# Kernel optimization log

Hardware: AMD Instinct MI355X
Metric: run time of the kernel (lower is better)

Reference implementation:

```python
import jax, jax.numpy as jnp
import numpy as np

MOMENTUM = 0.9
BN_EPS = 1e-5
NORM_EPS = 1e-12
NUM_CLASSES = 10000
DIM_MLP = 512
NUM_EXPERTS = 3
FEAT_DIM = 256
N = 4096


def _l2norm(x, axis=-1):
    # F.normalize: x / max(||x||, eps)
    n = jnp.sqrt(jnp.sum(x * x, axis=axis, keepdims=True))
    return x / jnp.maximum(n, NORM_EPS)


def setup_inputs() -> dict:
    key = jax.random.key(0)
    ks = jax.random.split(key, 8)
    feat_in = jax.random.normal(ks[0], (N, DIM_MLP * NUM_EXPERTS), dtype=jnp.float32)
    label = jax.random.randint(ks[1], (N,), 0, NUM_CLASSES, dtype=jnp.int32)
    # encoder params
    W1 = jax.random.normal(ks[2], (DIM_MLP * NUM_EXPERTS, DIM_MLP), dtype=jnp.float32) / np.sqrt(DIM_MLP * NUM_EXPERTS)
    b1 = jnp.zeros((DIM_MLP,), dtype=jnp.float32)
    gamma = jnp.ones((DIM_MLP,), dtype=jnp.float32)
    beta = jnp.zeros((DIM_MLP,), dtype=jnp.float32)
    W2 = jax.random.normal(ks[3], (DIM_MLP, FEAT_DIM), dtype=jnp.float32) / np.sqrt(DIM_MLP)
    b2 = jnp.zeros((FEAT_DIM,), dtype=jnp.float32)
    # memory bank buffer: randn then row-normalized (as in __init__)
    memory_pt = _l2norm(jax.random.normal(ks[4], (NUM_CLASSES, FEAT_DIM), dtype=jnp.float32))
    return {"feat_in": feat_in, "label": label, "W1": W1, "b1": b1,
            "gamma": gamma, "beta": beta, "W2": W2, "b2": b2,
            "memory_pt": memory_pt}


def _encoder(feat_in, W1, b1, gamma, beta, W2, b2):
    h = feat_in @ W1 + b1                       # [N, dim_mlp]
    # BatchNorm1d in training mode: batch statistics (biased variance)
    mu = jnp.mean(h, axis=0)
    var = jnp.mean((h - mu) ** 2, axis=0)
    h = (h - mu) * jax.lax.rsqrt(var + BN_EPS) * gamma + beta
    h = jax.nn.relu(h)
    out = h @ W2 + b2                           # [N, 256]
    return _l2norm(out, axis=1)


def _update_memory(memory_pt, feat, label):
    # Strictly sequential per-sample momentum update (order matters for
    # duplicate labels), each touched row renormalized — lax.scan recurrence.
    def step(mem, xy):
        x, y = xy
        pt = MOMENTUM * mem[y] + (1.0 - MOMENTUM) * x
        pt = _l2norm(pt, axis=0)
        return mem.at[y].set(pt), None
    mem, _ = jax.lax.scan(step, memory_pt, (feat, label))
    return mem


def reference(feat_in, label, W1, b1, gamma, beta, W2, b2, memory_pt):
    feat = _encoder(feat_in, W1, b1, gamma, beta, W2, b2)   # [N, 256], unit rows
    # memory_pt.detach(): no grad flows through the memory bank
    mem = _update_memory(jax.lax.stop_gradient(memory_pt),
                         jax.lax.stop_gradient(feat), label)
    mem = jax.lax.stop_gradient(mem)
    sim_logit = jnp.einsum('nc,kc->nk', feat, mem)          # [N, K]
    return sim_logit
```

## Files before the change

kernel.cpp:

```cpp
#include <hip/hip_runtime.h>
#include <stdint.h>

typedef _Float16 f16;
typedef _Float16 f16x2 __attribute__((ext_vector_type(2)));
typedef _Float16 f16x4 __attribute__((ext_vector_type(4)));
typedef _Float16 f16x8 __attribute__((ext_vector_type(8)));
typedef float f32x4 __attribute__((ext_vector_type(4)));

typedef __attribute__((address_space(1))) void gvoid;
typedef __attribute__((address_space(3))) void lvoid;

#define NROWS 4096
#define DIMIN 1536
#define DMLP 512
#define FDIM 256
#define NCLS 10000
#define NPAD 10112
#define NBMW 320

__device__ __forceinline__ void load_lds16(const void* g, void* l) {
    __builtin_amdgcn_global_load_lds((gvoid*)g, (lvoid*)l, 16, 0, 0);
}

template<int TM, int TN, bool STATS, bool NT>
__global__ __launch_bounds__(256) void gemm_t(
    const f16* __restrict__ A, const f16* __restrict__ Bt,
    float* __restrict__ C, const float* __restrict__ bias,
    int K, int ldc, int Nstore,
    float* __restrict__ sums, float* __restrict__ sqs)
{
    constexpr int BK = 64;
    constexpr int AM = TM / 32;
    constexpr int AN = TN / 32;
    constexpr int CA = TM * 8;
    constexpr int CB = TN * 8;
    constexpr int RTOT = (CA + CB) / 256;
    constexpr int SPAN = (TM + TN) * BK;
    static_assert(CA % 256 == 0, "A/B staging split must be round-aligned");

    __shared__ f16 smem[2 * SPAN];

    const int tid  = threadIdx.x;
    const int lane = tid & 63;
    const int w    = tid >> 6;
    const int wm   = (w >> 1) * (TM / 2);
    const int wn   = (w & 1) * (TN / 2);
    const int row0 = blockIdx.x * TM;
    const int col0 = blockIdx.y * TN;
    const int quad = lane >> 4;
    const int r16  = lane & 15;

    f32x4 acc[AM][AN] = {};

    const f16* gsrc[RTOT];
    int ldsoff[RTOT];
#pragma unroll
    for (int r = 0; r < RTOT; ++r) {
        int c = tid + r * 256;
        bool isA = (c < CA);
        int cc = isA ? c : c - CA;
        int row = cc >> 3;
        int gs = (cc & 7) ^ (row & 7);
        gsrc[r] = (isA ? A + (size_t)(row0 + row) * K
                       : Bt + (size_t)(col0 + row) * K) + gs * 8;
        ldsoff[r] = (isA ? 0 : TM * BK) + cc * 8;
    }

    const int nt = K / BK;

#pragma unroll
    for (int r = 0; r < RTOT; ++r)
        load_lds16(gsrc[r], smem + ldsoff[r]);
    __syncthreads();

    int buf = 0;
    for (int t = 0; t < nt; ++t) {
        if (t + 1 < nt) {
            const int k0 = (t + 1) * BK;
            const int o = (buf ^ 1) * SPAN;
#pragma unroll
            for (int r = 0; r < RTOT; ++r)
                load_lds16(gsrc[r] + k0, smem + o + ldsoff[r]);
        }
        const f16* As = smem + buf * SPAN;
        const f16* Bs = As + TM * BK;
#pragma unroll
        for (int ks = 0; ks < 2; ++ks) {
            f16x8 af[AM], bq[AN];
#pragma unroll
            for (int mi = 0; mi < AM; ++mi) {
                int row = wm + mi * 16 + r16;
                int slot = (ks * 4 + quad) ^ (r16 & 7);
                af[mi] = *(const f16x8*)&As[row * BK + slot * 8];
            }
#pragma unroll
            for (int ni = 0; ni < AN; ++ni) {
                int row = wn + ni * 16 + r16;
                int slot = (ks * 4 + quad) ^ (r16 & 7);
                bq[ni] = *(const f16x8*)&Bs[row * BK + slot * 8];
            }
#pragma unroll
            for (int mi = 0; mi < AM; ++mi)
#pragma unroll
                for (int ni = 0; ni < AN; ++ni)
                    acc[mi][ni] = __builtin_amdgcn_mfma_f32_16x16x32_f16(
                        af[mi], bq[ni], acc[mi][ni], 0, 0, 0);
        }
        __syncthreads();
        buf ^= 1;
    }

#pragma unroll
    for (int ni = 0; ni < AN; ++ni) {
        int col = col0 + wn + ni * 16 + r16;
        float bv = bias ? bias[col] : 0.0f;
        float s = 0.0f, q = 0.0f;
        if (col < Nstore) {
#pragma unroll
            for (int mi = 0; mi < AM; ++mi) {
                int rowb = row0 + wm + mi * 16 + quad * 4;
#pragma unroll
                for (int r = 0; r < 4; ++r) {
                    float v = acc[mi][ni][r] + bv;
                    if constexpr (NT)
                        __builtin_nontemporal_store(v, &C[(size_t)(rowb + r) * ldc + col]);
                    else
                        C[(size_t)(rowb + r) * ldc + col] = v;
                    if constexpr (STATS) { s += v; q += v * v; }
                }
            }
        }
        if constexpr (STATS) {
            s += __shfl_xor(s, 16); s += __shfl_xor(s, 32);
            q += __shfl_xor(q, 16); q += __shfl_xor(q, 32);
            if (quad == 0) {
                atomicAdd(&sums[col], s);
                atomicAdd(&sqs[col], q);
            }
        }
    }
}

__global__ void zero_k(float* __restrict__ p, int n) {
    int i = blockIdx.x * 256 + threadIdx.x;
    if (i < n) p[i] = 0.0f;
}

__global__ void f32_to_f16_k(const float* __restrict__ in, f16* __restrict__ out, int n4) {
    int i = blockIdx.x * 256 + threadIdx.x;
    if (i >= n4) return;
    float4 v = *(const float4*)&in[(size_t)i * 4];
    f16x4 o = {(f16)v.x, (f16)v.y, (f16)v.z, (f16)v.w};
    *(f16x4*)&out[(size_t)i * 4] = o;
}

__global__ void transpose_f16_tile_k(const float* __restrict__ in, f16* __restrict__ out,
                                     int R, int C) {
    __shared__ float t[32][33];
    int tx = threadIdx.x & 31, ty = threadIdx.x >> 5;
    int c0 = blockIdx.x * 32, r0 = blockIdx.y * 32;
#pragma unroll
    for (int k = 0; k < 4; ++k)
        t[ty + k * 8][tx] = in[(size_t)(r0 + ty + k * 8) * C + c0 + tx];
    __syncthreads();
#pragma unroll
    for (int k = 0; k < 4; ++k)
        out[(size_t)(c0 + ty + k * 8) * R + r0 + tx] = (f16)t[tx][ty + k * 8];
}

__global__ void touch_k(const int* __restrict__ label, unsigned int* __restrict__ bm) {
    int i = blockIdx.x * 256 + threadIdx.x;
    int y = label[i];
    atomicOr(&bm[y >> 5], 1u << (y & 31));
}

__global__ void bn_finish_k(const float* __restrict__ sums, const float* __restrict__ sqs,
                            const float* __restrict__ gamma, const float* __restrict__ beta,
                            float* __restrict__ scale, float* __restrict__ shift) {
    int c = blockIdx.x * 256 + threadIdx.x;
    if (c >= DMLP) return;
    const float inv_n = 1.0f / 4096.0f;
    float mu = sums[c] * inv_n;
    float var = fmaxf(sqs[c] * inv_n - mu * mu, 0.0f);
    float a = rsqrtf(var + 1e-5f) * gamma[c];
    scale[c] = a;
    shift[c] = beta[c] - mu * a;
}

__global__ void bn_apply_k(const float* __restrict__ h, const float* __restrict__ scale,
                           const float* __restrict__ shift, f16* __restrict__ out) {
    int i = blockIdx.x * 256 + threadIdx.x;
    int c = (i & 127) * 4;
    float4 v = *(const float4*)&h[(size_t)i * 4];
    float4 sc = *(const float4*)&scale[c];
    float4 sh = *(const float4*)&shift[c];
    f16x4 o = {(f16)fmaxf(v.x * sc.x + sh.x, 0.0f),
               (f16)fmaxf(v.y * sc.y + sh.y, 0.0f),
               (f16)fmaxf(v.z * sc.z + sh.z, 0.0f),
               (f16)fmaxf(v.w * sc.w + sh.w, 0.0f)};
    *(f16x4*)&out[(size_t)i * 4] = o;
}

__global__ void l2norm_k(const float* __restrict__ X, float* __restrict__ Y, f16* __restrict__ Yh) {
    int wv = (blockIdx.x * 256 + threadIdx.x) >> 6;
    int lane = threadIdx.x & 63;
    float4 v = *(const float4*)&X[(size_t)wv * FDIM + lane * 4];
    float s = v.x * v.x + v.y * v.y + v.z * v.z + v.w * v.w;
#pragma unroll
    for (int off = 32; off > 0; off >>= 1) s += __shfl_xor(s, off);
    float inv = 1.0f / fmaxf(sqrtf(s), 1e-12f);
    float4 o = {v.x * inv, v.y * inv, v.z * inv, v.w * inv};
    *(float4*)&Y[(size_t)wv * FDIM + lane * 4] = o;
    f16x4 oh = {(f16)o.x, (f16)o.y, (f16)o.z, (f16)o.w};
    *(f16x4*)&Yh[(size_t)wv * FDIM + lane * 4] = oh;
}

__global__ void chain_k(const int* __restrict__ label, const float* __restrict__ feat,
                        const float* __restrict__ mp, const unsigned int* __restrict__ bm,
                        f16* __restrict__ memh) {
    int y = (blockIdx.x * 256 + threadIdx.x) >> 6;
    int lane = threadIdx.x & 63;
    float4 m = {0.f, 0.f, 0.f, 0.f};
    if (y < NCLS) {
        m = *(const float4*)&mp[(size_t)y * FDIM + lane * 4];
        if ((bm[y >> 5] >> (y & 31)) & 1u) {
            for (int g = 0; g < 64; ++g) {
                int lab = label[g * 64 + lane];
                unsigned long long mask = __ballot(lab == y);
                while (mask) {
                    int b = __builtin_ctzll(mask);
                    mask &= mask - 1;
                    int i = g * 64 + b;
                    float4 x = *(const float4*)&feat[(size_t)i * FDIM + lane * 4];
                    m.x = 0.9f * m.x + 0.1f * x.x;
                    m.y = 0.9f * m.y + 0.1f * x.y;
                    m.z = 0.9f * m.z + 0.1f * x.z;
                    m.w = 0.9f * m.w + 0.1f * x.w;
                    float s = m.x * m.x + m.y * m.y + m.z * m.z + m.w * m.w;
#pragma unroll
                    for (int off = 32; off > 0; off >>= 1) s += __shfl_xor(s, off);
                    float inv = 1.0f / fmaxf(sqrtf(s), 1e-12f);
                    m.x *= inv; m.y *= inv; m.z *= inv; m.w *= inv;
                }
            }
        }
    }
    f16x4 o = {(f16)m.x, (f16)m.y, (f16)m.z, (f16)m.w};
    *(f16x4*)&memh[(size_t)y * FDIM + lane * 4] = o;
}

extern "C" void kernel_launch(void* const* d_in, const int* in_sizes, int n_in,
                              void* d_out, int out_size, void* d_ws, size_t ws_size,
                              hipStream_t stream) {
    const float* feat_in = (const float*)d_in[0];
    const int*   label   = (const int*)d_in[1];
    const float* W1      = (const float*)d_in[2];
    const float* b1      = (const float*)d_in[3];
    const float* gamma   = (const float*)d_in[4];
    const float* beta    = (const float*)d_in[5];
    const float* W2      = (const float*)d_in[6];
    const float* b2      = (const float*)d_in[7];
    const float* mp      = (const float*)d_in[8];
    float* out = (float*)d_out;

    char* w = (char*)d_ws;
    f16* A1h   = (f16*)w;   w += (size_t)NROWS * DIMIN * 2;
    f16* W1t   = (f16*)w;   w += (size_t)DMLP * DIMIN * 2;
    f16* W2t   = (f16*)w;   w += (size_t)FDIM * DMLP * 2;
    float* h   = (float*)w; w += (size_t)NROWS * DMLP * 4;
    f16* h2    = (f16*)w;   w += (size_t)NROWS * DMLP * 2;
    float* out2= (float*)w; w += (size_t)NROWS * FDIM * 4;
    float* feat= (float*)w; w += (size_t)NROWS * FDIM * 4;
    f16* feath = (f16*)w;   w += (size_t)NROWS * FDIM * 2;
    f16* memh  = (f16*)w;   w += (size_t)NPAD * FDIM * 2;
    float* sums= (float*)w; w += DMLP * 4;
    float* sqs = (float*)w; w += DMLP * 4;
    unsigned int* bm = (unsigned int*)w; w += NBMW * 4;
    float* bnsc= (float*)w; w += DMLP * 4;
    float* bnsh= (float*)w; w += DMLP * 4;

    zero_k<<<6, 256, 0, stream>>>(sums, 2 * DMLP + NBMW);
    touch_k<<<NROWS / 256, 256, 0, stream>>>(label, bm);
    f32_to_f16_k<<<(NROWS * DIMIN / 4) / 256, 256, 0, stream>>>(feat_in, A1h, NROWS * DIMIN / 4);
    {
        dim3 g1(DMLP / 32, DIMIN / 32);
        transpose_f16_tile_k<<<g1, 256, 0, stream>>>(W1, W1t, DIMIN, DMLP);
        dim3 g2(FDIM / 32, DMLP / 32);
        transpose_f16_tile_k<<<g2, 256, 0, stream>>>(W2, W2t, DMLP, FDIM);
    }

    {
        dim3 g(NROWS / 128, DMLP / 64);
        gemm_t<128, 64, true, false><<<g, 256, 0, stream>>>(
            A1h, W1t, h, b1, DIMIN, DMLP, DMLP, sums, sqs);
    }

    bn_finish_k<<<2, 256, 0, stream>>>(sums, sqs, gamma, beta, bnsc, bnsh);
    bn_apply_k<<<(NROWS * DMLP / 4) / 256, 256, 0, stream>>>(h, bnsc, bnsh, h2);

    {
        dim3 g(NROWS / 64, FDIM / 64);
        gemm_t<64, 64, false, false><<<g, 256, 0, stream>>>(
            h2, W2t, out2, b2, DMLP, FDIM, FDIM, nullptr, nullptr);
    }

    l2norm_k<<<NROWS / 4, 256, 0, stream>>>(out2, feat, feath);

    chain_k<<<NPAD / 4, 256, 0, stream>>>(label, feat, mp, bm, memh);

    {
        dim3 g(NROWS / 128, NPAD / 128);
        gemm_t<128, 128, false, true><<<g, 256, 0, stream>>>(
            feath, memh, out, nullptr, FDIM, NCLS, NCLS, nullptr, nullptr);
    }
}
```

Measured before the change: 295.1 us.

## Fuse setup kernels, fold BN finish into apply, vectorize final GEMM stores

Merges the zeroing, label-bitmap, f32-to-f16 conversion and both weight transposes into one multi-role setup kernel, with the bitmap built in LDS. Folds the BN scale/shift computation into the apply kernel, dropping one launch and a small buffer. Swaps the MFMA operand order in the large similarity GEMM so each lane holds four consecutive columns, allowing 16-byte vector nontemporal stores instead of scalar strided ones. The single-block bitmap role serializes the 4096 label atomics in one workgroup, and the per-thread BN stat recomputation adds some redundant math.

Result: no change. 293.3 us (-0.6%).

```diff
diff --git a/kernel.cpp b/kernel.cpp
--- a/kernel.cpp
+++ b/kernel.cpp
@@ -2,7 +2,6 @@
 #include <stdint.h>
 
 typedef _Float16 f16;
-typedef _Float16 f16x2 __attribute__((ext_vector_type(2)));
 typedef _Float16 f16x4 __attribute__((ext_vector_type(4)));
 typedef _Float16 f16x8 __attribute__((ext_vector_type(8)));
 typedef float f32x4 __attribute__((ext_vector_type(4)));
@@ -22,7 +21,7 @@
     __builtin_amdgcn_global_load_lds((gvoid*)g, (lvoid*)l, 16, 0, 0);
 }
 
-template<int TM, int TN, bool STATS, bool NT>
+template<int TM, int TN, bool STATS, bool NT, bool SWAP>
 __global__ __launch_bounds__(256) void gemm_t(
     const f16* __restrict__ A, const f16* __restrict__ Bt,
     float* __restrict__ C, const float* __restrict__ bias,
@@ -37,6 +36,7 @@
     constexpr int RTOT = (CA + CB) / 256;
     constexpr int SPAN = (TM + TN) * BK;
     static_assert(CA % 256 == 0, "A/B staging split must be round-aligned");
+    static_assert(!(SWAP && STATS), "SWAP epilogue has no STATS path");
 
     __shared__ f16 smem[2 * SPAN];
 
@@ -102,98 +102,145 @@
 #pragma unroll
             for (int mi = 0; mi < AM; ++mi)
 #pragma unroll
-                for (int ni = 0; ni < AN; ++ni)
-                    acc[mi][ni] = __builtin_amdgcn_mfma_f32_16x16x32_f16(
-                        af[mi], bq[ni], acc[mi][ni], 0, 0, 0);
+                for (int ni = 0; ni < AN; ++ni) {
+                    if constexpr (SWAP)
+                        acc[mi][ni] = __builtin_amdgcn_mfma_f32_16x16x32_f16(
+                            bq[ni], af[mi], acc[mi][ni], 0, 0, 0);
+                    else
+                        acc[mi][ni] = __builtin_amdgcn_mfma_f32_16x16x32_f16(
+                            af[mi], bq[ni], acc[mi][ni], 0, 0, 0);
+                }
         }
         __syncthreads();
         buf ^= 1;
     }
 
-#pragma unroll
-    for (int ni = 0; ni < AN; ++ni) {
-        int col = col0 + wn + ni * 16 + r16;
-        float bv = bias ? bias[col] : 0.0f;
-        float s = 0.0f, q = 0.0f;
-        if (col < Nstore) {
-#pragma unroll
-            for (int mi = 0; mi < AM; ++mi) {
-                int rowb = row0 + wm + mi * 16 + quad * 4;
-#pragma unroll
-                for (int r = 0; r < 4; ++r) {
-                    float v = acc[mi][ni][r] + bv;
+    if constexpr (SWAP) {
+#pragma unroll
+        for (int ni = 0; ni < AN; ++ni) {
+            int c0 = col0 + wn + ni * 16 + quad * 4;
+            if (c0 < Nstore) {
+#pragma unroll
+                for (int mi = 0; mi < AM; ++mi) {
+                    int m = row0 + wm + mi * 16 + r16;
                     if constexpr (NT)
-                        __builtin_nontemporal_store(v, &C[(size_t)(rowb + r) * ldc + col]);
+                        __builtin_nontemporal_store(acc[mi][ni],
+                            (f32x4*)&C[(size_t)m * ldc + c0]);
                     else
-                        C[(size_t)(rowb + r) * ldc + col] = v;
-                    if constexpr (STATS) { s += v; q += v * v; }
-                }
-            }
-        }
-        if constexpr (STATS) {
-            s += __shfl_xor(s, 16); s += __shfl_xor(s, 32);
-            q += __shfl_xor(q, 16); q += __shfl_xor(q, 32);
-            if (quad == 0) {
-                atomicAdd(&sums[col], s);
-                atomicAdd(&sqs[col], q);
-            }
-        }
-    }
-}
-
-__global__ void zero_k(float* __restrict__ p, int n) {
-    int i = blockIdx.x * 256 + threadIdx.x;
-    if (i < n) p[i] = 0.0f;
-}
-
-__global__ void f32_to_f16_k(const float* __restrict__ in, f16* __restrict__ out, int n4) {
-    int i = blockIdx.x * 256 + threadIdx.x;
-    if (i >= n4) return;
-    float4 v = *(const float4*)&in[(size_t)i * 4];
-    f16x4 o = {(f16)v.x, (f16)v.y, (f16)v.z, (f16)v.w};
-    *(f16x4*)&out[(size_t)i * 4] = o;
-}
-
-__global__ void transpose_f16_tile_k(const float* __restrict__ in, f16* __restrict__ out,
-                                     int R, int C) {
-    __shared__ float t[32][33];
-    int tx = threadIdx.x & 31, ty = threadIdx.x >> 5;
-    int c0 = blockIdx.x * 32, r0 = blockIdx.y * 32;
+                        *(f32x4*)&C[(size_t)m * ldc + c0] = acc[mi][ni];
+                }
+            }
+        }
+    } else {
+#pragma unroll
+        for (int ni = 0; ni < AN; ++ni) {
+            int col = col0 + wn + ni * 16 + r16;
+            float bv = bias ? bias[col] : 0.0f;
+            float s = 0.0f, q = 0.0f;
+            if (col < Nstore) {
+#pragma unroll
+                for (int mi = 0; mi < AM; ++mi) {
+                    int rowb = row0 + wm + mi * 16 + quad * 4;
+#pragma unroll
+                    for (int r = 0; r < 4; ++r) {
+                        float v = acc[mi][ni][r] + bv;
+                        if constexpr (NT)
+                            __builtin_nontemporal_store(v, &C[(size_t)(rowb + r) * ldc + col]);
+                        else
+                            C[(size_t)(rowb + r) * ldc + col] = v;
+                        if constexpr (STATS) { s += v; q += v * v; }
+                    }
+                }
+            }
+            if constexpr (STATS) {
+                s += __shfl_xor(s, 16); s += __shfl_xor(s, 32);
+                q += __shfl_xor(q, 16); q += __shfl_xor(q, 32);
+                if (quad == 0) {
+                    atomicAdd(&sums[col], s);
+                    atomicAdd(&sqs[col], q);
+                }
+            }
+        }
+    }
+}
+
+__device__ __forceinline__ void transpose_tile(
+    const float* __restrict__ in, f16* __restrict__ out,
+    int R, int C, int bxx, int byy, float* t, int tid)
+{
+    int tx = tid & 31, ty = tid >> 5;
+    int c0 = bxx * 32, r0 = byy * 32;
 #pragma unroll
     for (int k = 0; k < 4; ++k)
-        t[ty + k * 8][tx] = in[(size_t)(r0 + ty + k * 8) * C + c0 + tx];
+        t[(ty + k * 8) * 33 + tx] = in[(size_t)(r0 + ty + k * 8) * C + c0 + tx];
     __syncthreads();
 #pragma unroll
     for (int k = 0; k < 4; ++k)
-        out[(size_t)(c0 + ty + k * 8) * R + r0 + tx] = (f16)t[tx][ty + k * 8];
-}
-
-__global__ void touch_k(const int* __restrict__ label, unsigned int* __restrict__ bm) {
-    int i = blockIdx.x * 256 + threadIdx.x;
-    int y = label[i];
-    atomicOr(&bm[y >> 5], 1u << (y & 31));
-}
-
-__global__ void bn_finish_k(const float* __restrict__ sums, const float* __restrict__ sqs,
-                            const float* __restrict__ gamma, const float* __restrict__ beta,
-                            float* __restrict__ scale, float* __restrict__ shift) {
-    int c = blockIdx.x * 256 + threadIdx.x;
-    if (c >= DMLP) return;
-    const float inv_n = 1.0f / 4096.0f;
-    float mu = sums[c] * inv_n;
-    float var = fmaxf(sqs[c] * inv_n - mu * mu, 0.0f);
-    float a = rsqrtf(var + 1e-5f) * gamma[c];
-    scale[c] = a;
-    shift[c] = beta[c] - mu * a;
-}
-
-__global__ void bn_apply_k(const float* __restrict__ h, const float* __restrict__ scale,
-                           const float* __restrict__ shift, f16* __restrict__ out) {
+        out[(size_t)(c0 + ty + k * 8) * R + r0 + tx] = (f16)t[tx * 33 + ty + k * 8];
+}
+
+__global__ void setup_k(const float* __restrict__ feat_in, f16* __restrict__ A1h,
+                        const float* __restrict__ W1, f16* __restrict__ W1t,
+                        const float* __restrict__ W2, f16* __restrict__ W2t,
+                        const int* __restrict__ label, float* __restrict__ stats,
+                        unsigned int* __restrict__ bm)
+{
+    __shared__ float t[32 * 33];
+    const int b = blockIdx.x, tid = threadIdx.x;
+    if (b < 6144) {
+        int i = b * 256 + tid;
+        float4 v = *(const float4*)&feat_in[(size_t)i * 4];
+        f16x4 o = {(f16)v.x, (f16)v.y, (f16)v.z, (f16)v.w};
+        *(f16x4*)&A1h[(size_t)i * 4] = o;
+    } else if (b < 6912) {
+        int idx = b - 6144;
+        transpose_tile(W1, W1t, DIMIN, DMLP, idx & 15, idx >> 4, t, tid);
+    } else if (b < 7040) {
+        int idx = b - 6912;
+        transpose_tile(W2, W2t, DMLP, FDIM, idx & 7, idx >> 3, t, tid);
+    } else {
+        unsigned int* lbm = (unsigned int*)t;
+        for (int i = tid; i < NBMW; i += 256) lbm[i] = 0u;
+        for (int i = tid; i < 2 * DMLP; i += 256) stats[i] = 0.0f;
+        __syncthreads();
+        for (int i = tid; i < NROWS; i += 256) {
+            int y = label[i];
+            atomicOr(&lbm[y >> 5], 1u << (y & 31));
+        }
+        __syncthreads();
+        for (int i = tid; i < NBMW; i += 256) bm[i] = lbm[i];
+    }
+}
+
+__global__ void bn_apply_k(const float* __restrict__ h,
+                           const float* __restrict__ sums, const float* __restrict__ sqs,
+                           const float* __restrict__ gamma, const float* __restrict__ beta,
+                           f16* __restrict__ out) {
     int i = blockIdx.x * 256 + threadIdx.x;
     int c = (i & 127) * 4;
+    const float inv_n = 1.0f / 4096.0f;
+    float4 s4 = *(const float4*)&sums[c];
+    float4 q4 = *(const float4*)&sqs[c];
+    float4 g4 = *(const float4*)&gamma[c];
+    float4 b4 = *(const float4*)&beta[c];
+    float4 sc, sh;
+    {
+        float mu = s4.x * inv_n, var = fmaxf(q4.x * inv_n - mu * mu, 0.0f);
+        float a = rsqrtf(var + 1e-5f) * g4.x; sc.x = a; sh.x = b4.x - mu * a;
+    }
+    {
+        float mu = s4.y * inv_n, var = fmaxf(q4.y * inv_n - mu * mu, 0.0f);
+        float a = rsqrtf(var + 1e-5f) * g4.y; sc.y = a; sh.y = b4.y - mu * a;
+    }
+    {
+        float mu = s4.z * inv_n, var = fmaxf(q4.z * inv_n - mu * mu, 0.0f);
+        float a = rsqrtf(var + 1e-5f) * g4.z; sc.z = a; sh.z = b4.z - mu * a;
+    }
+    {
+        float mu = s4.w * inv_n, var = fmaxf(q4.w * inv_n - mu * mu, 0.0f);
+        float a = rsqrtf(var + 1e-5f) * g4.w; sc.w = a; sh.w = b4.w - mu * a;
+    }
     float4 v = *(const float4*)&h[(size_t)i * 4];
-    float4 sc = *(const float4*)&scale[c];
-    float4 sh = *(const float4*)&shift[c];
     f16x4 o = {(f16)fmaxf(v.x * sc.x + sh.x, 0.0f),
                (f16)fmaxf(v.y * sc.y + sh.y, 0.0f),
                (f16)fmaxf(v.z * sc.z + sh.z, 0.0f),
@@ -276,31 +323,22 @@
     float* sums= (float*)w; w += DMLP * 4;
     float* sqs = (float*)w; w += DMLP * 4;
     unsigned int* bm = (unsigned int*)w; w += NBMW * 4;
-    float* bnsc= (float*)w; w += DMLP * 4;
-    float* bnsh= (float*)w; w += DMLP * 4;
-
-    zero_k<<<6, 256, 0, stream>>>(sums, 2 * DMLP + NBMW);
-    touch_k<<<NROWS / 256, 256, 0, stream>>>(label, bm);
-    f32_to_f16_k<<<(NROWS * DIMIN / 4) / 256, 256, 0, stream>>>(feat_in, A1h, NROWS * DIMIN / 4);
-    {
-        dim3 g1(DMLP / 32, DIMIN / 32);
-        transpose_f16_tile_k<<<g1, 256, 0, stream>>>(W1, W1t, DIMIN, DMLP);
-        dim3 g2(FDIM / 32, DMLP / 32);
-        transpose_f16_tile_k<<<g2, 256, 0, stream>>>(W2, W2t, DMLP, FDIM);
-    }
+
+    setup_k<<<7041, 256, 0, stream>>>(feat_in, A1h, W1, W1t, W2, W2t,
+                                      label, sums, bm);
 
     {
         dim3 g(NROWS / 128, DMLP / 64);
-        gemm_t<128, 64, true, false><<<g, 256, 0, stream>>>(
+        gemm_t<128, 64, true, false, false><<<g, 256, 0, stream>>>(
             A1h, W1t, h, b1, DIMIN, DMLP, DMLP, sums, sqs);
     }
 
-    bn_finish_k<<<2, 256, 0, stream>>>(sums, sqs, gamma, beta, bnsc, bnsh);
-    bn_apply_k<<<(NROWS * DMLP / 4) / 256, 256, 0, stream>>>(h, bnsc, bnsh, h2);
+    bn_apply_k<<<(NROWS * DMLP / 4) / 256, 256, 0, stream>>>(
+        h, sums, sqs, gamma, beta, h2);
 
     {
         dim3 g(NROWS / 64, FDIM / 64);
-        gemm_t<64, 64, false, false><<<g, 256, 0, stream>>>(
+        gemm_t<64, 64, false, false, false><<<g, 256, 0, stream>>>(
             h2, W2t, out2, b2, DMLP, FDIM, FDIM, nullptr, nullptr);
     }
 
@@ -310,7 +348,7 @@
 
     {
         dim3 g(NROWS / 128, NPAD / 128);
-        gemm_t<128, 128, false, true><<<g, 256, 0, stream>>>(
+        gemm_t<128, 128, false, true, true><<<g, 256, 0, stream>>>(
             feath, memh, out, nullptr, FDIM, NCLS, NCLS, nullptr, nullptr);
     }
 }
```
